# Performance work log

Measured on AMD Instinct MI355X. Metric: run time of the kernel, lower is better.

Reference implementation:

```python
import jax, jax.numpy as jnp
import numpy as np

N = 50000   # nodes
E = 800000  # edges
D = 200     # h_dim == out_dim
R = 500     # num_rels
L = 2       # num_hidden_layers
RRELU_SLOPE = (1.0 / 8.0 + 1.0 / 3.0) / 2.0  # eval-mode F.rrelu negative slope


def _rrelu(x):
    return jnp.where(x >= 0, x, x * jnp.float32(RRELU_SLOPE))


def setup_inputs() -> dict:
    key = jax.random.key(0)
    ks = jax.random.split(key, 10)
    s = np.float32(1.0 / np.sqrt(D))  # ~xavier scale
    return {
        "init_ent_emb": jax.random.normal(ks[0], (N, D), jnp.float32),
        "rel_emb": jax.random.normal(ks[1], (R, D), jnp.float32),
        "weight_neighbor": jax.random.normal(ks[2], (L, D, D), jnp.float32) * s,
        "loop_weight": jax.random.normal(ks[3], (L, D, D), jnp.float32) * s,
        "evolve_loop_weight": jax.random.normal(ks[4], (L, D, D), jnp.float32) * s,
        "norm": jax.random.uniform(ks[5], (N, 1), jnp.float32),
        "src": jax.random.randint(ks[6], (E,), 0, N, dtype=jnp.int32),
        "dst": jax.random.randint(ks[7], (E,), 0, N, dtype=jnp.int32),
        "etype": jax.random.randint(ks[8], (E,), 0, R, dtype=jnp.int32),
        "node_id": jnp.arange(N, dtype=jnp.int32),
    }


def reference(init_ent_emb, rel_emb, weight_neighbor, loop_weight,
              evolve_loop_weight, norm, src, dst, etype, node_id):
    # g.ndata['h'] = init_ent_emb[node_id]
    h = init_ent_emb[node_id]                                    # [N, D]
    # mask of nodes with in-degree > 0 (fixed across layers)
    indeg = jnp.zeros((N,), jnp.float32).at[dst].add(1.0)
    has_in = (indeg > 0)[:, None]                                # [N, 1]
    for l in range(L):
        # loop message: loop_weight where in-degree>0, evolve_loop_weight otherwise
        loop_msg = jnp.where(has_in,
                             h @ loop_weight[l],
                             h @ evolve_loop_weight[l])          # [N, D]
        # per-edge message: (h_src + rel_emb[etype]) @ W_neighbor
        msg = (h[src] + rel_emb[etype]) @ weight_neighbor[l]     # [E, D]
        # sum-scatter to destination nodes, then per-node norm (apply_func)
        agg = jax.ops.segment_sum(msg, dst, num_segments=N)      # [N, D]
        h = _rrelu(agg * norm + loop_msg)
    return h
```

## Files before the change

### kernel.cpp

```cpp
#include <hip/hip_runtime.h>

#define D 200
#define RRELU_SLOPE 0.22916666666666666f
#define STRIDE 96
#define PAD 8
#define EPT 8

typedef unsigned short u16;
typedef unsigned int u32;

using bf16x8 = __attribute__((ext_vector_type(8))) short;
using f32x4  = __attribute__((ext_vector_type(4))) float;
using f32x2  = __attribute__((ext_vector_type(2))) float;

__device__ __forceinline__ float rrelu(float x) {
    return x >= 0.0f ? x : x * RRELU_SLOPE;
}
__device__ __forceinline__ float bf2f(u32 u) {
    union { u32 i; float f; } c; c.i = u << 16; return c.f;
}
__device__ __forceinline__ u32 f2bf(float f) {
    union { float f; u32 i; } c; c.f = f;
    return (c.i + 0x7fffu + ((c.i >> 16) & 1u)) >> 16;
}
__device__ __forceinline__ u32 pack2(float x, float y) {
    return f2bf(x) | (f2bf(y) << 16);
}
__device__ __forceinline__ void gll16(const void* g, void* l) {
    __builtin_amdgcn_global_load_lds((const __attribute__((address_space(1))) void*)g,
                                     (__attribute__((address_space(3))) void*)l,
                                     16, 0, 0);
}

__device__ __forceinline__ void accw(u32 w, f32x2& acc) {
    union { u32 i; float f; } lo, hi;
    lo.i = w << 16;
    hi.i = w & 0xffff0000u;
    f32x2 t; t[0] = lo.f; t[1] = hi.f;
    acc += t;
}
__device__ __forceinline__ void accq(uint4 q, f32x2* a) {
    accw(q.x, a[0]); accw(q.y, a[1]); accw(q.z, a[2]); accw(q.w, a[3]);
}


__global__ void front_k(const float* __restrict__ rel, const float* __restrict__ Wn,
                        const float* __restrict__ Wl, u16* __restrict__ relb,
                        u16* __restrict__ Bt, u16* __restrict__ hb0d,
                        u16* __restrict__ hb1d, int* __restrict__ noin_cnt,
                        const int* __restrict__ dst, const int* __restrict__ src,
                        const int* __restrict__ etype, int* __restrict__ cnt,
                        u32* __restrict__ ep, int E,
                        const float* __restrict__ init, const int* __restrict__ nid,
                        u16* __restrict__ hb, int N,
                        int prepB, int scatB) {
    int b = blockIdx.x;
    if (b < prepB) {
        int i = b * blockDim.x + threadIdx.x;
        if (i == 0) *noin_cnt = 0;
        if (i < 200) { hb0d[i] = 0; hb1d[i] = 0; }
        if (i < 100200) relb[i] = (i < 100000) ? (u16)f2bf(rel[i]) : (u16)0;
        if (i < 2 * 256 * 416) {
            int l = i / (256 * 416);
            int rem = i % (256 * 416);
            int c = rem / 416;
            int k = rem % 416;
            float v = 0.0f;
            if (c < 200 && k < 400)
                v = (k < 200) ? Wn[(size_t)l * 40000 + k * 200 + c]
                              : Wl[(size_t)l * 40000 + (k - 200) * 200 + c];
            Bt[i] = (u16)f2bf(v);
        }
    } else if (b < prepB + scatB) {
        int base = ((b - prepB) * blockDim.x + threadIdx.x) * EPT;
        if (base + EPT <= E) {
            int4 d0 = *(const int4*)(dst + base);
            int4 d1 = *(const int4*)(dst + base + 4);
            int4 s0 = *(const int4*)(src + base);
            int4 s1 = *(const int4*)(src + base + 4);
            int4 t0 = *(const int4*)(etype + base);
            int4 t1 = *(const int4*)(etype + base + 4);
            int dd[8] = {d0.x, d0.y, d0.z, d0.w, d1.x, d1.y, d1.z, d1.w};
            int ss[8] = {s0.x, s0.y, s0.z, s0.w, s1.x, s1.y, s1.z, s1.w};
            int tt[8] = {t0.x, t0.y, t0.z, t0.w, t1.x, t1.y, t1.z, t1.w};
            int cc[8];
#pragma unroll
            for (int j = 0; j < 8; ++j) cc[j] = atomicAdd(&cnt[dd[j]], 1);
#pragma unroll
            for (int j = 0; j < 8; ++j)
                if (cc[j] < STRIDE)
                    ep[(size_t)dd[j] * STRIDE + cc[j]] = (u32)ss[j] | ((u32)tt[j] << 17);
        } else {
            for (int j = 0; j < EPT; ++j) {
                int e = base + j;
                if (e < E) {
                    int d = dst[e];
                    int c = atomicAdd(&cnt[d], 1);
                    if (c < STRIDE)
                        ep[(size_t)d * STRIDE + c] = (u32)src[e] | ((u32)etype[e] << 17);
                }
            }
        }
    } else {
        int lane = threadIdx.x & 63;
        int v = (b - prepB - scatB) * 4 + (threadIdx.x >> 6);
        if (v >= N || lane >= 50) return;
        float4 f = *(const float4*)(init + (size_t)nid[v] * D + lane * 4);
        uint2 o;
        o.x = pack2(f.x, f.y);
        o.y = pack2(f.z, f.w);
        *(uint2*)(hb + (size_t)v * D + lane * 4) = o;
    }
}


__global__ __launch_bounds__(256) void gagg0_k(
        const u16* __restrict__ hb, const u16* __restrict__ relb,
        const u32* __restrict__ ep, const int* __restrict__ cnt,
        const float* __restrict__ norm,
        u16* __restrict__ aggb, u16* __restrict__ relsumb,
        int* __restrict__ noin, int* __restrict__ noin_cnt, int N, u32 dummy) {
    int lane = threadIdx.x & 63;
    int wave = threadIdx.x >> 6;
    int li = lane & 31;
    int v = blockIdx.x * 8 + wave * 2 + (lane >> 5);
    if (v >= N || li >= 25) return;
    size_t lo = (size_t)li * 8;
    const u16* hbL = hb + lo;
    const u16* rbL = relb + lo;
    int c = cnt[v];
    if (c > STRIDE) c = STRIDE;
    if (li == 0 && c == 0) noin[atomicAdd(noin_cnt, 1)] = v;
    int rv = (c + PAD - 1) >> 3;
    const u32* pp = ep + (size_t)v * STRIDE;
    f32x2 a[4] = {}, rr[4] = {};
    u32 p[8];
    uint4 qh[8];
#pragma unroll
    for (int j = 0; j < 8; ++j) p[j] = (j < c) ? pp[j] : dummy;
#pragma unroll
    for (int j = 0; j < 8; ++j)
        qh[j] = *(const uint4*)(hbL + (size_t)(p[j] & 0x1FFFFu) * D);
    for (int r = 0; r < rv; ++r) {
        int nb = (r + 1) * 8;
        u32 pn[8];
#pragma unroll
        for (int j = 0; j < 8; ++j)
            pn[j] = (nb + j < c) ? pp[nb + j] : dummy;
        uint4 qr[8];
#pragma unroll
        for (int j = 0; j < 8; ++j)
            qr[j] = *(const uint4*)(rbL + (size_t)((p[j] >> 17) & 0x3FFu) * D);
#pragma unroll
        for (int j = 0; j < 8; ++j) accq(qh[j], a);
#pragma unroll
        for (int j = 0; j < 8; ++j)
            qh[j] = *(const uint4*)(hbL + (size_t)(pn[j] & 0x1FFFFu) * D);
#pragma unroll
        for (int j = 0; j < 8; ++j) accq(qr[j], rr);
#pragma unroll
        for (int j = 0; j < 8; ++j) p[j] = pn[j];
    }
    uint4 rs;
    rs.x = pack2(rr[0][0], rr[0][1]); rs.y = pack2(rr[1][0], rr[1][1]);
    rs.z = pack2(rr[2][0], rr[2][1]); rs.w = pack2(rr[3][0], rr[3][1]);
    *(uint4*)(relsumb + (size_t)v * D + lo) = rs;
    float nv = norm[v];
    uint4 o;
    o.x = pack2((a[0][0] + rr[0][0]) * nv, (a[0][1] + rr[0][1]) * nv);
    o.y = pack2((a[1][0] + rr[1][0]) * nv, (a[1][1] + rr[1][1]) * nv);
    o.z = pack2((a[2][0] + rr[2][0]) * nv, (a[2][1] + rr[2][1]) * nv);
    o.w = pack2((a[3][0] + rr[3][0]) * nv, (a[3][1] + rr[3][1]) * nv);
    *(uint4*)(aggb + (size_t)v * D + lo) = o;
}


__global__ __launch_bounds__(256) void gagg1_k(
        const u16* __restrict__ hb, const u32* __restrict__ ep,
        const int* __restrict__ cnt, const float* __restrict__ norm,
        const u16* __restrict__ addb, u16* __restrict__ outb, int N, u32 dummy) {
    int lane = threadIdx.x & 63;
    int wave = threadIdx.x >> 6;
    int li = lane & 31;
    int v = blockIdx.x * 8 + wave * 2 + (lane >> 5);
    if (v >= N || li >= 25) return;
    size_t lo = (size_t)li * 8;
    const u16* hbL = hb + lo;
    int c = cnt[v];
    if (c > STRIDE) c = STRIDE;
    int rv = (c + PAD - 1) >> 3;
    const u32* pp = ep + (size_t)v * STRIDE;
    f32x2 a[4] = {};
    u32 p[8];
    uint4 qh[8];
#pragma unroll
    for (int j = 0; j < 8; ++j) p[j] = (j < c) ? pp[j] : dummy;
#pragma unroll
    for (int j = 0; j < 8; ++j)
        qh[j] = *(const uint4*)(hbL + (size_t)(p[j] & 0x1FFFFu) * D);
    for (int r = 0; r < rv; ++r) {
        int nb = (r + 1) * 8;
        u32 pn[8];
#pragma unroll
        for (int j = 0; j < 8; ++j)
            pn[j] = (nb + j < c) ? pp[nb + j] : dummy;
#pragma unroll
        for (int j = 0; j < 8; ++j) accq(qh[j], a);
#pragma unroll
        for (int j = 0; j < 8; ++j)
            qh[j] = *(const uint4*)(hbL + (size_t)(pn[j] & 0x1FFFFu) * D);
#pragma unroll
        for (int j = 0; j < 8; ++j) p[j] = pn[j];
    }
    {
        uint4 q = *(const uint4*)(addb + (size_t)v * D + lo);
        accq(q, a);
    }
    float nv = norm[v];
    uint4 o;
    o.x = pack2(a[0][0] * nv, a[0][1] * nv);
    o.y = pack2(a[1][0] * nv, a[1][1] * nv);
    o.z = pack2(a[2][0] * nv, a[2][1] * nv);
    o.w = pack2(a[3][0] * nv, a[3][1] * nv);
    *(uint4*)(outb + (size_t)v * D + lo) = o;
}


__global__ __launch_bounds__(256) void gemm_k(
        const u16* __restrict__ Aagg, const u16* __restrict__ Ah,
        const u16* __restrict__ Bt,
        float* __restrict__ outF, u16* __restrict__ outB, int M) {
    __shared__ __align__(16) u16 As[2][64 * 32];
    __shared__ __align__(16) u16 Bs[2][256 * 32];
    int tid = threadIdx.x;
    int lane = tid & 63;
    int wave = tid >> 6;
    int rowBase = blockIdx.x * 64;
    int m = lane & 15;
    int kq = (lane >> 4) * 8;

    int srow = tid >> 2;
    int kg = (tid & 3) * 8;
    size_t aRow = (size_t)(rowBase + srow);

    f32x4 acc[4][4] = {};

    auto stage = [&](int buf, int k0) {
        int k = k0 + kg;
        const u16* gA = (k < 200) ? Aagg + aRow * D + k
                                  : Ah + aRow * D + (k - 200);
        gll16(gA, &As[buf][0] + wave * 512);
#pragma unroll
        for (int p = 0; p < 4; ++p) {
            const u16* gB = Bt + (size_t)(p * 64 + srow) * 416 + k;
            gll16(gB, &Bs[buf][0] + p * 2048 + wave * 512);
        }
    };

    stage(0, 0);
    __syncthreads();

    int cur = 0;
    for (int t = 0; t < 13; ++t) {
        if (t < 12) stage(cur ^ 1, (t + 1) * 32);

        const u16* A = &As[cur][0];
        const u16* B = &Bs[cur][0];
        bf16x8 a0 = *(const bf16x8*)(A + (m) * 32 + kq);
        bf16x8 a1 = *(const bf16x8*)(A + (16 + m) * 32 + kq);
        bf16x8 a2 = *(const bf16x8*)(A + (32 + m) * 32 + kq);
        bf16x8 a3 = *(const bf16x8*)(A + (48 + m) * 32 + kq);
        int wc = wave * 64;
        bf16x8 b0 = *(const bf16x8*)(B + (wc + m) * 32 + kq);
        bf16x8 b1 = *(const bf16x8*)(B + (wc + 16 + m) * 32 + kq);
        bf16x8 b2 = *(const bf16x8*)(B + (wc + 32 + m) * 32 + kq);
        bf16x8 b3 = *(const bf16x8*)(B + (wc + 48 + m) * 32 + kq);
        acc[0][0] = __builtin_amdgcn_mfma_f32_16x16x32_bf16(a0, b0, acc[0][0], 0, 0, 0);
        acc[0][1] = __builtin_amdgcn_mfma_f32_16x16x32_bf16(a0, b1, acc[0][1], 0, 0, 0);
        acc[0][2] = __builtin_amdgcn_mfma_f32_16x16x32_bf16(a0, b2, acc[0][2], 0, 0, 0);
        acc[0][3] = __builtin_amdgcn_mfma_f32_16x16x32_bf16(a0, b3, acc[0][3], 0, 0, 0);
        acc[1][0] = __builtin_amdgcn_mfma_f32_16x16x32_bf16(a1, b0, acc[1][0], 0, 0, 0);
        acc[1][1] = __builtin_amdgcn_mfma_f32_16x16x32_bf16(a1, b1, acc[1][1], 0, 0, 0);
        acc[1][2] = __builtin_amdgcn_mfma_f32_16x16x32_bf16(a1, b2, acc[1][2], 0, 0, 0);
        acc[1][3] = __builtin_amdgcn_mfma_f32_16x16x32_bf16(a1, b3, acc[1][3], 0, 0, 0);
        acc[2][0] = __builtin_amdgcn_mfma_f32_16x16x32_bf16(a2, b0, acc[2][0], 0, 0, 0);
        acc[2][1] = __builtin_amdgcn_mfma_f32_16x16x32_bf16(a2, b1, acc[2][1], 0, 0, 0);
        acc[2][2] = __builtin_amdgcn_mfma_f32_16x16x32_bf16(a2, b2, acc[2][2], 0, 0, 0);
        acc[2][3] = __builtin_amdgcn_mfma_f32_16x16x32_bf16(a2, b3, acc[2][3], 0, 0, 0);
        acc[3][0] = __builtin_amdgcn_mfma_f32_16x16x32_bf16(a3, b0, acc[3][0], 0, 0, 0);
        acc[3][1] = __builtin_amdgcn_mfma_f32_16x16x32_bf16(a3, b1, acc[3][1], 0, 0, 0);
        acc[3][2] = __builtin_amdgcn_mfma_f32_16x16x32_bf16(a3, b2, acc[3][2], 0, 0, 0);
        acc[3][3] = __builtin_amdgcn_mfma_f32_16x16x32_bf16(a3, b3, acc[3][3], 0, 0, 0);

        __syncthreads();
        cur ^= 1;
    }

    int cRow = (lane >> 4) * 4;
    int cCol = lane & 15;
#pragma unroll
    for (int i = 0; i < 4; ++i) {
#pragma unroll
        for (int j = 0; j < 4; ++j) {
            int col = wave * 64 + j * 16 + cCol;
            if (col >= 200) continue;
#pragma unroll
            for (int r = 0; r < 4; ++r) {
                int row = rowBase + i * 16 + cRow + r;
                if (row < M) {
                    float val = rrelu(acc[i][j][r]);
                    if (outF) outF[(size_t)row * D + col] = val;
                    if (outB) outB[(size_t)row * D + col] = (u16)f2bf(val);
                }
            }
        }
    }
}


__global__ void fixup_k(const u16* __restrict__ hb, const float* __restrict__ We,
                        const int* __restrict__ noin, const int* __restrict__ noin_cnt,
                        float* __restrict__ outF, u16* __restrict__ outB) {
    int cnt = *noin_cnt;
    for (int i = blockIdx.x; i < cnt; i += gridDim.x) {
        int v = noin[i];
        int j = threadIdx.x;
        if (j < D) {
            float acc = 0.0f;
            for (int k = 0; k < D; ++k)
                acc += bf2f(hb[(size_t)v * D + k]) * We[(size_t)k * D + j];
            float r = rrelu(acc);
            if (outF) outF[(size_t)v * D + j] = r;
            if (outB) outB[(size_t)v * D + j] = (u16)f2bf(r);
        }
    }
}

extern "C" void kernel_launch(void* const* d_in, const int* in_sizes, int n_in,
                              void* d_out, int out_size, void* d_ws, size_t ws_size,
                              hipStream_t stream) {
    const float* init  = (const float*)d_in[0];
    const float* rel   = (const float*)d_in[1];
    const float* Wn    = (const float*)d_in[2];
    const float* Wl    = (const float*)d_in[3];
    const float* We    = (const float*)d_in[4];
    const float* norm  = (const float*)d_in[5];
    const int* src     = (const int*)d_in[6];
    const int* dst     = (const int*)d_in[7];
    const int* etype   = (const int*)d_in[8];
    const int* node_id = (const int*)d_in[9];
    float* out = (float*)d_out;

    int N = in_sizes[5];
    int E = in_sizes[6];
    size_t NP = (size_t)N + 256;

    char* w = (char*)d_ws;
    auto carve = [&](size_t bytes) {
        char* p = w;
        w += (bytes + 255) & ~(size_t)255;
        return p;
    };
    u16* hb0     = (u16*)carve(NP * D * sizeof(u16));
    u16* hb1     = (u16*)carve(NP * D * sizeof(u16));
    u16* aggb    = (u16*)carve(NP * D * sizeof(u16));
    u16* relsumb = (u16*)carve((size_t)N * D * sizeof(u16));
    u16* relb    = (u16*)carve((size_t)501 * D * sizeof(u16));
    u16* Bt      = (u16*)carve((size_t)2 * 256 * 416 * sizeof(u16));
    int* cnt     = (int*)carve((size_t)N * sizeof(int));
    u32* epack   = (u32*)carve(((size_t)N * STRIDE + PAD) * sizeof(u32));
    int* noin    = (int*)carve((size_t)N * sizeof(int));
    int* noin_cnt = (int*)carve(sizeof(int));

    (void)hipMemsetAsync(cnt, 0, (size_t)N * sizeof(int), stream);

    int prepN = 2 * 256 * 416;
    int prepB = (prepN + 255) / 256;
    int scatB = (E + 256 * EPT - 1) / (256 * EPT);
    int gathB = (N + 3) / 4;
    front_k<<<prepB + scatB + gathB, 256, 0, stream>>>(
        rel, Wn, Wl, relb, Bt,
        hb0 + (size_t)N * D, hb1 + (size_t)N * D, noin_cnt,
        dst, src, etype, cnt, epack, E,
        init, node_id, hb0, N, prepB, scatB);

    u32 dummy = (u32)N | (500u << 17);
    int gemmBlocks = (N + 63) / 64;

    gagg0_k<<<(N + 7) / 8, 256, 0, stream>>>(hb0, relb, epack, cnt, norm,
                                             aggb, relsumb, noin, noin_cnt,
                                             N, dummy);
    gemm_k<<<gemmBlocks, 256, 0, stream>>>(aggb, hb0, Bt, nullptr, hb1, N);
    fixup_k<<<8, 256, 0, stream>>>(hb0, We, noin, noin_cnt, nullptr, hb1);

    gagg1_k<<<(N + 7) / 8, 256, 0, stream>>>(hb1, epack, cnt, norm,
                                             relsumb, aggb, N, dummy);
    gemm_k<<<gemmBlocks, 256, 0, stream>>>(aggb, hb1, Bt + 256 * 416, out, nullptr, N);
    fixup_k<<<8, 256, 0, stream>>>(hb1, We + D * D, noin, noin_cnt, out, nullptr);
}
```

Measured before the change: 346.0 us.

## Load GEMM fragments directly from global into registers, drop LDS staging

The GEMM kernel no longer stages A and B tiles through shared memory with global_load_lds and block barriers. Each wave now loads its MFMA operand fragments straight from global memory into registers, double-buffered across k-steps. This removes the LDS traffic and __syncthreads, but the four waves of a block each fetch the same A rows, and B is re-read per wave from L2 with less coalesced access, so it leans on cache hits and uses more registers.

```diff
diff --git a/kernel.cpp b/kernel.cpp
--- a/kernel.cpp
+++ b/kernel.cpp
@@ -25,11 +25,6 @@
 }
 __device__ __forceinline__ u32 pack2(float x, float y) {
     return f2bf(x) | (f2bf(y) << 16);
-}
-__device__ __forceinline__ void gll16(const void* g, void* l) {
-    __builtin_amdgcn_global_load_lds((const __attribute__((address_space(1))) void*)g,
-                                     (__attribute__((address_space(3))) void*)l,
-                                     16, 0, 0);
 }
 
 __device__ __forceinline__ void accw(u32 w, f32x2& acc) {
@@ -230,70 +225,48 @@
         const u16* __restrict__ Aagg, const u16* __restrict__ Ah,
         const u16* __restrict__ Bt,
         float* __restrict__ outF, u16* __restrict__ outB, int M) {
-    __shared__ __align__(16) u16 As[2][64 * 32];
-    __shared__ __align__(16) u16 Bs[2][256 * 32];
     int tid = threadIdx.x;
     int lane = tid & 63;
     int wave = tid >> 6;
     int rowBase = blockIdx.x * 64;
     int m = lane & 15;
     int kq = (lane >> 4) * 8;
-
-    int srow = tid >> 2;
-    int kg = (tid & 3) * 8;
-    size_t aRow = (size_t)(rowBase + srow);
+    int wc = wave * 64;
 
     f32x4 acc[4][4] = {};
 
-    auto stage = [&](int buf, int k0) {
-        int k = k0 + kg;
-        const u16* gA = (k < 200) ? Aagg + aRow * D + k
-                                  : Ah + aRow * D + (k - 200);
-        gll16(gA, &As[buf][0] + wave * 512);
-#pragma unroll
-        for (int p = 0; p < 4; ++p) {
-            const u16* gB = Bt + (size_t)(p * 64 + srow) * 416 + k;
-            gll16(gB, &Bs[buf][0] + p * 2048 + wave * 512);
+    auto loadA = [&](int k, bf16x8* a) {
+#pragma unroll
+        for (int i = 0; i < 4; ++i) {
+            size_t row = (size_t)(rowBase + i * 16 + m);
+            const u16* g = (k < 200) ? Aagg + row * D + k
+                                     : Ah + row * D + (k - 200);
+            a[i] = *(const bf16x8*)g;
         }
     };
-
-    stage(0, 0);
-    __syncthreads();
-
-    int cur = 0;
+    auto loadB = [&](int k, bf16x8* bfr) {
+#pragma unroll
+        for (int j = 0; j < 4; ++j)
+            bfr[j] = *(const bf16x8*)(Bt + (size_t)(wc + j * 16 + m) * 416 + k);
+    };
+
+    bf16x8 a0[4], b0[4], a1[4], b1[4];
+    loadA(kq, a0);
+    loadB(kq, b0);
     for (int t = 0; t < 13; ++t) {
-        if (t < 12) stage(cur ^ 1, (t + 1) * 32);
-
-        const u16* A = &As[cur][0];
-        const u16* B = &Bs[cur][0];
-        bf16x8 a0 = *(const bf16x8*)(A + (m) * 32 + kq);
-        bf16x8 a1 = *(const bf16x8*)(A + (16 + m) * 32 + kq);
-        bf16x8 a2 = *(const bf16x8*)(A + (32 + m) * 32 + kq);
-        bf16x8 a3 = *(const bf16x8*)(A + (48 + m) * 32 + kq);
-        int wc = wave * 64;
-        bf16x8 b0 = *(const bf16x8*)(B + (wc + m) * 32 + kq);
-        bf16x8 b1 = *(const bf16x8*)(B + (wc + 16 + m) * 32 + kq);
-        bf16x8 b2 = *(const bf16x8*)(B + (wc + 32 + m) * 32 + kq);
-        bf16x8 b3 = *(const bf16x8*)(B + (wc + 48 + m) * 32 + kq);
-        acc[0][0] = __builtin_amdgcn_mfma_f32_16x16x32_bf16(a0, b0, acc[0][0], 0, 0, 0);
-        acc[0][1] = __builtin_amdgcn_mfma_f32_16x16x32_bf16(a0, b1, acc[0][1], 0, 0, 0);
-        acc[0][2] = __builtin_amdgcn_mfma_f32_16x16x32_bf16(a0, b2, acc[0][2], 0, 0, 0);
-        acc[0][3] = __builtin_amdgcn_mfma_f32_16x16x32_bf16(a0, b3, acc[0][3], 0, 0, 0);
-        acc[1][0] = __builtin_amdgcn_mfma_f32_16x16x32_bf16(a1, b0, acc[1][0], 0, 0, 0);
-        acc[1][1] = __builtin_amdgcn_mfma_f32_16x16x32_bf16(a1, b1, acc[1][1], 0, 0, 0);
-        acc[1][2] = __builtin_amdgcn_mfma_f32_16x16x32_bf16(a1, b2, acc[1][2], 0, 0, 0);
-        acc[1][3] = __builtin_amdgcn_mfma_f32_16x16x32_bf16(a1, b3, acc[1][3], 0, 0, 0);
-        acc[2][0] = __builtin_amdgcn_mfma_f32_16x16x32_bf16(a2, b0, acc[2][0], 0, 0, 0);
-        acc[2][1] = __builtin_amdgcn_mfma_f32_16x16x32_bf16(a2, b1, acc[2][1], 0, 0, 0);
-        acc[2][2] = __builtin_amdgcn_mfma_f32_16x16x32_bf16(a2, b2, acc[2][2], 0, 0, 0);
-        acc[2][3] = __builtin_amdgcn_mfma_f32_16x16x32_bf16(a2, b3, acc[2][3], 0, 0, 0);
-        acc[3][0] = __builtin_amdgcn_mfma_f32_16x16x32_bf16(a3, b0, acc[3][0], 0, 0, 0);
-        acc[3][1] = __builtin_amdgcn_mfma_f32_16x16x32_bf16(a3, b1, acc[3][1], 0, 0, 0);
-        acc[3][2] = __builtin_amdgcn_mfma_f32_16x16x32_bf16(a3, b2, acc[3][2], 0, 0, 0);
-        acc[3][3] = __builtin_amdgcn_mfma_f32_16x16x32_bf16(a3, b3, acc[3][3], 0, 0, 0);
-
-        __syncthreads();
-        cur ^= 1;
+        if (t < 12) {
+            int kn = (t + 1) * 32 + kq;
+            loadA(kn, a1);
+            loadB(kn, b1);
+        }
+#pragma unroll
+        for (int i = 0; i < 4; ++i)
+#pragma unroll
+            for (int j = 0; j < 4; ++j)
+                acc[i][j] = __builtin_amdgcn_mfma_f32_16x16x32_bf16(
+                    a0[i], b0[j], acc[i][j], 0, 0, 0);
+#pragma unroll
+        for (int i = 0; i < 4; ++i) { a0[i] = a1[i]; b0[i] = b1[i]; }
     }
 
     int cRow = (lane >> 4) * 4;
@@ -302,7 +275,7 @@
     for (int i = 0; i < 4; ++i) {
 #pragma unroll
         for (int j = 0; j < 4; ++j) {
-            int col = wave * 64 + j * 16 + cCol;
+            int col = wc + j * 16 + cCol;
             if (col >= 200) continue;
 #pragma unroll
             for (int r = 0; r < 4; ++r) {
```

Result: no change. 351.2 us (+1.5%).
